# Optimization experiments

Hardware: AMD Instinct MI355X
Metric: run time of the kernel (lower is better)

The kernel has to match this reference:

```python
import jax, jax.numpy as jnp
import numpy as np


def setup_inputs() -> dict:
    key = jax.random.key(0)
    k1, k2 = jax.random.split(key)
    N, D, C = 65536, 512, 64
    embeddings = jax.random.normal(k1, (N, D), dtype=jnp.float32)
    labels = jax.random.randint(k2, (N,), 0, C, dtype=jnp.int64)
    return {"embeddings": embeddings, "labels": labels, "num_classes": C}


def reference(embeddings, labels, num_classes):
    # Per-class mean (prototypes) via segment reductions. Labels are assumed
    # to be 0..C-1 with all classes present, so unique(labels) == arange(C)
    # and local_labels == labels (faithful to the torch loop in that regime).
    ones = jnp.ones(labels.shape, dtype=embeddings.dtype)
    counts = jax.ops.segment_sum(ones, labels, num_segments=num_classes)  # [C]
    sums = jax.ops.segment_sum(embeddings, labels, num_segments=num_classes)  # [C, D]
    prototypes = sums / counts[:, None]

    # Euclidean cdist: ||e||^2 + ||p||^2 - 2 e.p^T, clamped for numerical safety
    e2 = jnp.sum(embeddings * embeddings, axis=1, keepdims=True)  # [N, 1]
    p2 = jnp.sum(prototypes * prototypes, axis=1)  # [C]
    cross = embeddings @ prototypes.T  # [N, C]
    d2 = jnp.maximum(e2 + p2[None, :] - 2.0 * cross, 1e-12)
    logits = -jnp.sqrt(d2)  # [N, C], negative distances

    log_probs = jax.nn.log_softmax(logits, axis=1)
    n = labels.shape[0]
    nll = -log_probs[jnp.arange(n), labels]
    loss = jnp.mean(nll)
    accuracy = jnp.mean((jnp.argmax(logits, axis=1) == labels).astype(jnp.float32))
    return (loss, accuracy)
```

## Files before the change

### kernel.cpp

```cpp
#include <hip/hip_runtime.h>
#include <math.h>

#define NROWS 65536
#define DIM   512
#define NCLS  64
#define CCAP  1280

typedef __attribute__((ext_vector_type(4))) float f32x4;
typedef __attribute__((ext_vector_type(8))) short s16x8;

#define WS_PROTOSUM 0
#define WS_CURSORS  32768
#define WS_LOSS     32832
#define WS_ACC      32833
#define WS_P2       32836
#define WS_PERM     32912
#define WS_PB       32912
#define MEMSET_WORDS 32834

static __device__ __forceinline__ unsigned short f2bf(float f) {
    unsigned int u = __float_as_uint(f);
    u += 0x7FFF + ((u >> 16) & 1);
    return (unsigned short)(u >> 16);
}
static __device__ __forceinline__ float bf2f(unsigned short h) {
    return __uint_as_float(((unsigned int)h) << 16);
}

__global__ __launch_bounds__(256) void k_scatter(const int* __restrict__ labels,
                                                 int* __restrict__ cursors,
                                                 int* __restrict__ perm) {
    __shared__ int lh[NCLS], lb[NCLS];
    int t = threadIdx.x;
    if (t < NCLS) lh[t] = 0;
    __syncthreads();
    int i = blockIdx.x * 256 + t;
    int lab = labels[i];
    int rank = atomicAdd(&lh[lab], 1);
    __syncthreads();
    if (t < NCLS) lb[t] = atomicAdd(&cursors[t], lh[t]);
    __syncthreads();
    int pos = lb[lab] + rank;
    if (pos < CCAP) perm[lab * CCAP + pos] = i;
}

__global__ __launch_bounds__(256) void k_psum(const float* __restrict__ emb,
                                              const int* __restrict__ cursors,
                                              const int* __restrict__ perm,
                                              float* __restrict__ protoSum) {
    __shared__ int permS[CCAP];
    __shared__ float2 red[256];
    int t   = threadIdx.x;
    int c   = blockIdx.x >> 5;
    int sub = blockIdx.x & 31;
    int dc  = sub & 3;
    int rs  = sub >> 2;
    int tl  = t & 63;
    int g   = t >> 6;

    int cnt = cursors[c];
    int n = (cnt < CCAP) ? cnt : CCAP;
    for (int i = t; i < n; i += 256) permS[i] = perm[c * CCAP + i];
    __syncthreads();

    const float2* eb = (const float2*)emb + dc * 64 + tl;
    float2 acc; acc.x = 0.f; acc.y = 0.f;
#pragma unroll 4
    for (int i = rs * 4 + g; i < n; i += 32) {
        int r = permS[i];
        float2 v = eb[(size_t)r * 256];
        acc.x += v.x; acc.y += v.y;
    }
    red[t] = acc;
    __syncthreads();
    if (t < 64) {
        float2 a = red[t], b = red[t + 64], cc = red[t + 128], d = red[t + 192];
        float sx = a.x + b.x + cc.x + d.x;
        float sy = a.y + b.y + cc.y + d.y;
        atomicAdd(&protoSum[(size_t)c * DIM + dc * 128 + t * 2], sx);
        atomicAdd(&protoSum[(size_t)c * DIM + dc * 128 + t * 2 + 1], sy);
    }
}

__global__ __launch_bounds__(512) void k_protofin(const float* __restrict__ protoSum,
                                                  const int* __restrict__ cursors,
                                                  unsigned short* __restrict__ pB,
                                                  float* __restrict__ p2) {
    int c = blockIdx.x, d = threadIdx.x;
    float mean = protoSum[(size_t)c * DIM + d] / (float)cursors[c];
    unsigned short mb = f2bf(mean);
    pB[(size_t)c * DIM + d] = mb;
    float mf = bf2f(mb);
    float sq = mf * mf;
#pragma unroll
    for (int o = 32; o > 0; o >>= 1) sq += __shfl_down(sq, o, 64);
    __shared__ float red[8];
    if ((d & 63) == 0) red[d >> 6] = sq;
    __syncthreads();
    if (d == 0) {
        float ss = 0.f;
#pragma unroll
        for (int w = 0; w < 8; ++w) ss += red[w];
        p2[c] = ss;
    }
}

#define LROWS 64
__global__ __launch_bounds__(256) void k_logits(const float* __restrict__ emb,
                                                const int* __restrict__ labels,
                                                const unsigned short* __restrict__ pB,
                                                const float* __restrict__ p2,
                                                float* __restrict__ lossAcc,
                                                float* __restrict__ accAcc) {
    __shared__ __align__(16) unsigned short Asm[LROWS * 36];
    __shared__ float e2s[LROWS];
    __shared__ float rb[8];

    int t    = threadIdx.x;
    int lane = t & 63;
    int wv   = t >> 6;
    int quad = lane >> 4;
    int l15  = lane & 15;
    int rbase = blockIdx.x * LROWS;

    f32x4 acc[4];
#pragma unroll
    for (int nt = 0; nt < 4; ++nt) acc[nt] = (f32x4){0.f, 0.f, 0.f, 0.f};
    float e2a0 = 0.f, e2a1 = 0.f;

    const float4* emb4 = (const float4*)(emb + (size_t)rbase * DIM);
    int row0 = t >> 3, j0 = t & 7;
    int row1 = 32 + row0;

    float4 g0 = emb4[(size_t)row0 * 128 + j0];
    float4 g1 = emb4[(size_t)row1 * 128 + j0];

    for (int kc = 0; kc < 16; ++kc) {
        e2a0 += g0.x * g0.x + g0.y * g0.y + g0.z * g0.z + g0.w * g0.w;
        e2a1 += g1.x * g1.x + g1.y * g1.y + g1.z * g1.z + g1.w * g1.w;
        ushort4 h0, h1;
        h0.x = f2bf(g0.x); h0.y = f2bf(g0.y); h0.z = f2bf(g0.z); h0.w = f2bf(g0.w);
        h1.x = f2bf(g1.x); h1.y = f2bf(g1.y); h1.z = f2bf(g1.z); h1.w = f2bf(g1.w);
        *(ushort4*)&Asm[row0 * 36 + j0 * 4] = h0;
        *(ushort4*)&Asm[row1 * 36 + j0 * 4] = h1;
        __syncthreads();

        s16x8 bf[4];
#pragma unroll
        for (int nt = 0; nt < 4; ++nt)
            bf[nt] = *(const s16x8*)(pB + (size_t)(nt * 16 + l15) * DIM + kc * 32 + quad * 8);
        s16x8 a = *(const s16x8*)&Asm[(wv * 16 + l15) * 36 + quad * 8];
        if (kc + 1 < 16) {
            g0 = emb4[(size_t)row0 * 128 + (kc + 1) * 8 + j0];
            g1 = emb4[(size_t)row1 * 128 + (kc + 1) * 8 + j0];
        }
        __syncthreads();
#pragma unroll
        for (int nt = 0; nt < 4; ++nt)
            acc[nt] = __builtin_amdgcn_mfma_f32_16x16x32_bf16(a, bf[nt], acc[nt], 0, 0, 0);
    }

    float v0 = e2a0;
    v0 += __shfl_xor(v0, 1, 64); v0 += __shfl_xor(v0, 2, 64); v0 += __shfl_xor(v0, 4, 64);
    float v1 = e2a1;
    v1 += __shfl_xor(v1, 1, 64); v1 += __shfl_xor(v1, 2, 64); v1 += __shfl_xor(v1, 4, 64);
    if ((lane & 7) == 0) {
        e2s[wv * 8 + (lane >> 3)]      = v0;
        e2s[32 + wv * 8 + (lane >> 3)] = v1;
    }
    __syncthreads();

    float nlls = 0.f, corr = 0.f;
#pragma unroll
    for (int reg = 0; reg < 4; ++reg) {
        int rloc = wv * 16 + quad * 4 + reg;
        float e2v = e2s[rloc];
        float lg[4];
#pragma unroll
        for (int nt = 0; nt < 4; ++nt) {
            float d2 = e2v + p2[nt * 16 + l15] - 2.f * acc[nt][reg];
            d2 = fmaxf(d2, 1e-12f);
            lg[nt] = -sqrtf(d2);
        }
        float mv = lg[0]; int mc = l15;
#pragma unroll
        for (int nt = 1; nt < 4; ++nt) {
            int cix = nt * 16 + l15;
            if (lg[nt] > mv) { mv = lg[nt]; mc = cix; }
        }
#pragma unroll
        for (int o = 1; o < 16; o <<= 1) {
            float mo = __shfl_xor(mv, o, 64);
            int   co = __shfl_xor(mc, o, 64);
            if (mo > mv || (mo == mv && co < mc)) { mv = mo; mc = co; }
        }
        int lab = labels[rbase + rloc];
        float se = 0.f, ll = 0.f;
#pragma unroll
        for (int nt = 0; nt < 4; ++nt) se += __expf(lg[nt] - mv);
        if ((lab & 15) == l15) ll = lg[lab >> 4];
#pragma unroll
        for (int o = 1; o < 16; o <<= 1) {
            se += __shfl_xor(se, o, 64);
            ll += __shfl_xor(ll, o, 64);
        }
        if (l15 == 0) {
            nlls += __logf(se) + mv - ll;
            corr += (mc == lab) ? 1.f : 0.f;
        }
    }
#pragma unroll
    for (int o = 1; o < 64; o <<= 1) {
        nlls += __shfl_xor(nlls, o, 64);
        corr += __shfl_xor(corr, o, 64);
    }
    if (lane == 0) { rb[wv] = nlls; rb[4 + wv] = corr; }
    __syncthreads();
    if (t == 0) {
        atomicAdd(lossAcc, rb[0] + rb[1] + rb[2] + rb[3]);
        atomicAdd(accAcc, rb[4] + rb[5] + rb[6] + rb[7]);
    }
}

__global__ void k_final(const float* __restrict__ lossAcc,
                        const float* __restrict__ accAcc,
                        float* __restrict__ out) {
    if (threadIdx.x == 0 && blockIdx.x == 0) {
        out[0] = lossAcc[0] * (1.f / NROWS);
        out[1] = accAcc[0] * (1.f / NROWS);
    }
}

extern "C" void kernel_launch(void* const* d_in, const int* in_sizes, int n_in,
                              void* d_out, int out_size, void* d_ws, size_t ws_size,
                              hipStream_t stream) {
    const float* emb    = (const float*)d_in[0];
    const int*   labels = (const int*)d_in[1];
    float* out = (float*)d_out;

    float* wsf = (float*)d_ws;
    int*   wsi = (int*)d_ws;
    float*          protoSum = wsf + WS_PROTOSUM;
    int*            cursors  = wsi + WS_CURSORS;
    float*          lossAcc  = wsf + WS_LOSS;
    float*          accAcc   = wsf + WS_ACC;
    float*          p2       = wsf + WS_P2;
    int*            perm     = wsi + WS_PERM;
    unsigned short* pB       = (unsigned short*)(wsf + WS_PB);

    hipMemsetAsync(d_ws, 0, MEMSET_WORDS * sizeof(int), stream);

    k_scatter<<<NROWS / 256, 256, 0, stream>>>(labels, cursors, perm);
    k_psum<<<NCLS * 32, 256, 0, stream>>>(emb, cursors, perm, protoSum);
    k_protofin<<<NCLS, 512, 0, stream>>>(protoSum, cursors, pB, p2);
    k_logits<<<NROWS / LROWS, 256, 0, stream>>>(emb, labels, pB, p2, lossAcc, accAcc);
    k_final<<<1, 64, 0, stream>>>(lossAcc, accAcc, out);
}
```

Measured before the change: 273.6 us.

## Load MFMA operands directly from global, widen psum loads, fuse final kernel

After: 309.3 us. 1.13x slower.

```diff
diff --git a/kernel.cpp b/kernel.cpp
--- a/kernel.cpp
+++ b/kernel.cpp
@@ -13,10 +13,11 @@
 #define WS_CURSORS  32768
 #define WS_LOSS     32832
 #define WS_ACC      32833
+#define WS_DONE     32834
 #define WS_P2       32836
 #define WS_PERM     32912
 #define WS_PB       32912
-#define MEMSET_WORDS 32834
+#define MEMSET_WORDS 32835
 
 static __device__ __forceinline__ unsigned short f2bf(float f) {
     unsigned int u = __float_as_uint(f);
@@ -49,36 +50,42 @@
                                               const int* __restrict__ perm,
                                               float* __restrict__ protoSum) {
     __shared__ int permS[CCAP];
-    __shared__ float2 red[256];
+    __shared__ float4 red[256];
     int t   = threadIdx.x;
     int c   = blockIdx.x >> 5;
     int sub = blockIdx.x & 31;
     int dc  = sub & 3;
     int rs  = sub >> 2;
-    int tl  = t & 63;
-    int g   = t >> 6;
+    int tl  = t & 31;
+    int g   = t >> 5;
 
     int cnt = cursors[c];
     int n = (cnt < CCAP) ? cnt : CCAP;
     for (int i = t; i < n; i += 256) permS[i] = perm[c * CCAP + i];
     __syncthreads();
 
-    const float2* eb = (const float2*)emb + dc * 64 + tl;
-    float2 acc; acc.x = 0.f; acc.y = 0.f;
+    const float4* eb = (const float4*)emb + dc * 32 + tl;
+    float4 acc = make_float4(0.f, 0.f, 0.f, 0.f);
 #pragma unroll 4
-    for (int i = rs * 4 + g; i < n; i += 32) {
+    for (int i = rs * 8 + g; i < n; i += 64) {
         int r = permS[i];
-        float2 v = eb[(size_t)r * 256];
-        acc.x += v.x; acc.y += v.y;
+        float4 v = eb[(size_t)r * 128];
+        acc.x += v.x; acc.y += v.y; acc.z += v.z; acc.w += v.w;
     }
     red[t] = acc;
     __syncthreads();
-    if (t < 64) {
-        float2 a = red[t], b = red[t + 64], cc = red[t + 128], d = red[t + 192];
-        float sx = a.x + b.x + cc.x + d.x;
-        float sy = a.y + b.y + cc.y + d.y;
-        atomicAdd(&protoSum[(size_t)c * DIM + dc * 128 + t * 2], sx);
-        atomicAdd(&protoSum[(size_t)c * DIM + dc * 128 + t * 2 + 1], sy);
+    if (t < 32) {
+        float4 s = red[t];
+#pragma unroll
+        for (int gg = 1; gg < 8; ++gg) {
+            float4 v = red[gg * 32 + t];
+            s.x += v.x; s.y += v.y; s.z += v.z; s.w += v.w;
+        }
+        float* dst = &protoSum[(size_t)c * DIM + dc * 128 + t * 4];
+        atomicAdd(dst + 0, s.x);
+        atomicAdd(dst + 1, s.y);
+        atomicAdd(dst + 2, s.z);
+        atomicAdd(dst + 3, s.w);
     }
 }
 
@@ -106,13 +113,15 @@
 }
 
 #define LROWS 64
+#define LGRID (NROWS / LROWS)
 __global__ __launch_bounds__(256) void k_logits(const float* __restrict__ emb,
                                                 const int* __restrict__ labels,
                                                 const unsigned short* __restrict__ pB,
                                                 const float* __restrict__ p2,
                                                 float* __restrict__ lossAcc,
-                                                float* __restrict__ accAcc) {
-    __shared__ __align__(16) unsigned short Asm[LROWS * 36];
+                                                float* __restrict__ accAcc,
+                                                unsigned int* __restrict__ doneCnt,
+                                                float* __restrict__ out) {
     __shared__ float e2s[LROWS];
     __shared__ float rb[8];
 
@@ -126,48 +135,34 @@
     f32x4 acc[4];
 #pragma unroll
     for (int nt = 0; nt < 4; ++nt) acc[nt] = (f32x4){0.f, 0.f, 0.f, 0.f};
-    float e2a0 = 0.f, e2a1 = 0.f;
-
-    const float4* emb4 = (const float4*)(emb + (size_t)rbase * DIM);
-    int row0 = t >> 3, j0 = t & 7;
-    int row1 = 32 + row0;
-
-    float4 g0 = emb4[(size_t)row0 * 128 + j0];
-    float4 g1 = emb4[(size_t)row1 * 128 + j0];
+    float e2a = 0.f;
+
+    const float4* arow = (const float4*)(emb + (size_t)(rbase + wv * 16 + l15) * DIM)
+                         + quad * 2;
+    const unsigned short* bbase = pB + (size_t)l15 * DIM + quad * 8;
 
     for (int kc = 0; kc < 16; ++kc) {
-        e2a0 += g0.x * g0.x + g0.y * g0.y + g0.z * g0.z + g0.w * g0.w;
-        e2a1 += g1.x * g1.x + g1.y * g1.y + g1.z * g1.z + g1.w * g1.w;
-        ushort4 h0, h1;
-        h0.x = f2bf(g0.x); h0.y = f2bf(g0.y); h0.z = f2bf(g0.z); h0.w = f2bf(g0.w);
-        h1.x = f2bf(g1.x); h1.y = f2bf(g1.y); h1.z = f2bf(g1.z); h1.w = f2bf(g1.w);
-        *(ushort4*)&Asm[row0 * 36 + j0 * 4] = h0;
-        *(ushort4*)&Asm[row1 * 36 + j0 * 4] = h1;
-        __syncthreads();
-
+        float4 a0 = arow[kc * 8 + 0];
+        float4 a1 = arow[kc * 8 + 1];
         s16x8 bf[4];
 #pragma unroll
         for (int nt = 0; nt < 4; ++nt)
-            bf[nt] = *(const s16x8*)(pB + (size_t)(nt * 16 + l15) * DIM + kc * 32 + quad * 8);
-        s16x8 a = *(const s16x8*)&Asm[(wv * 16 + l15) * 36 + quad * 8];
-        if (kc + 1 < 16) {
-            g0 = emb4[(size_t)row0 * 128 + (kc + 1) * 8 + j0];
-            g1 = emb4[(size_t)row1 * 128 + (kc + 1) * 8 + j0];
-        }
-        __syncthreads();
+            bf[nt] = *(const s16x8*)(bbase + (size_t)nt * 16 * DIM + kc * 32);
+        e2a += a0.x * a0.x + a0.y * a0.y + a0.z * a0.z + a0.w * a0.w;
+        e2a += a1.x * a1.x + a1.y * a1.y + a1.z * a1.z + a1.w * a1.w;
+        s16x8 af;
+        af[0] = (short)f2bf(a0.x); af[1] = (short)f2bf(a0.y);
+        af[2] = (short)f2bf(a0.z); af[3] = (short)f2bf(a0.w);
+        af[4] = (short)f2bf(a1.x); af[5] = (short)f2bf(a1.y);
+        af[6] = (short)f2bf(a1.z); af[7] = (short)f2bf(a1.w);
 #pragma unroll
         for (int nt = 0; nt < 4; ++nt)
-            acc[nt] = __builtin_amdgcn_mfma_f32_16x16x32_bf16(a, bf[nt], acc[nt], 0, 0, 0);
-    }
-
-    float v0 = e2a0;
-    v0 += __shfl_xor(v0, 1, 64); v0 += __shfl_xor(v0, 2, 64); v0 += __shfl_xor(v0, 4, 64);
-    float v1 = e2a1;
-    v1 += __shfl_xor(v1, 1, 64); v1 += __shfl_xor(v1, 2, 64); v1 += __shfl_xor(v1, 4, 64);
-    if ((lane & 7) == 0) {
-        e2s[wv * 8 + (lane >> 3)]      = v0;
-        e2s[32 + wv * 8 + (lane >> 3)] = v1;
-    }
+            acc[nt] = __builtin_amdgcn_mfma_f32_16x16x32_bf16(af, bf[nt], acc[nt], 0, 0, 0);
+    }
+
+    e2a += __shfl_xor(e2a, 16, 64);
+    e2a += __shfl_xor(e2a, 32, 64);
+    if (lane < 16) e2s[wv * 16 + lane] = e2a;
     __syncthreads();
 
     float nlls = 0.f, corr = 0.f;
@@ -219,15 +214,14 @@
     if (t == 0) {
         atomicAdd(lossAcc, rb[0] + rb[1] + rb[2] + rb[3]);
         atomicAdd(accAcc, rb[4] + rb[5] + rb[6] + rb[7]);
-    }
-}
-
-__global__ void k_final(const float* __restrict__ lossAcc,
-                        const float* __restrict__ accAcc,
-                        float* __restrict__ out) {
-    if (threadIdx.x == 0 && blockIdx.x == 0) {
-        out[0] = lossAcc[0] * (1.f / NROWS);
-        out[1] = accAcc[0] * (1.f / NROWS);
+        __threadfence();
+        unsigned int tk = atomicAdd(doneCnt, 1u);
+        if (tk == LGRID - 1) {
+            float ls = atomicAdd(lossAcc, 0.f);
+            float as_ = atomicAdd(accAcc, 0.f);
+            out[0] = ls * (1.f / NROWS);
+            out[1] = as_ * (1.f / NROWS);
+        }
     }
 }
 
@@ -244,6 +238,7 @@
     int*            cursors  = wsi + WS_CURSORS;
     float*          lossAcc  = wsf + WS_LOSS;
     float*          accAcc   = wsf + WS_ACC;
+    unsigned int*   doneCnt  = (unsigned int*)(wsi + WS_DONE);
     float*          p2       = wsf + WS_P2;
     int*            perm     = wsi + WS_PERM;
     unsigned short* pB       = (unsigned short*)(wsf + WS_PB);
@@ -253,6 +248,6 @@
     k_scatter<<<NROWS / 256, 256, 0, stream>>>(labels, cursors, perm);
     k_psum<<<NCLS * 32, 256, 0, stream>>>(emb, cursors, perm, protoSum);
     k_protofin<<<NCLS, 512, 0, stream>>>(protoSum, cursors, pB, p2);
-    k_logits<<<NROWS / LROWS, 256, 0, stream>>>(emb, labels, pB, p2, lossAcc, accAcc);
-    k_final<<<1, 64, 0, stream>>>(lossAcc, accAcc, out);
-}
+    k_logits<<<LGRID, 256, 0, stream>>>(emb, labels, pB, p2,
+                                        lossAcc, accAcc, doneCnt, out);
+}
```
